# Kernel optimization log

Measured on AMD Instinct MI355X. Metric: run time of the kernel, lower is better.

Reference implementation:

```python
import math
import jax, jax.numpy as jnp
import numpy as np

N, D, K = 8192, 256, 32


def setup_inputs() -> dict:
    key = jax.random.key(0)
    kx, kw, kb = jax.random.split(key, 3)
    x = jax.random.normal(kx, (N, D), dtype=jnp.float32)
    # params per _init_weights: w ~ N(1, 0.01), b ~ N(0, 0.01)
    w = 1.0 + 0.01 * jax.random.normal(kw, (K, D), dtype=jnp.float32)
    b = 0.01 * jax.random.normal(kb, (K, D), dtype=jnp.float32)
    return {"x": x, "w": w, "b": b}


def reference(x, w, b):
    # x: (N, D); w, b: (K, D)
    y1 = w[None, :, :] * (x[:, None, :] + b[None, :, :])        # (N, K, D)
    y2 = y1 * y1                                                 # (N, K, D)
    y4 = -0.5 * jnp.sum(y2, axis=-1)                             # (N, K)
    gamma = jax.nn.softmax(y4, axis=-1)                          # (N, K)
    y6 = (y2 - 1.0) * (1.0 / math.sqrt(2.0))                     # (N, K, D)
    g = gamma[:, :, None]                                        # (N, K, 1)
    n, kk, d = y1.shape
    sigma_part = (g * y6).reshape(n, kk * d)                     # (N, K*D)
    mu_part = (g * y1).reshape(n, kk * d)                        # (N, K*D)
    phi_patches = jnp.concatenate([sigma_part, mu_part], axis=-1)
    return jnp.mean(phi_patches, axis=0)                         # (2*K*D,)
```

## Files before the change

### kernel.cpp

```cpp
#include <hip/hip_runtime.h>
#include <math.h>

#define Nn 8192
#define Dd 256
#define Kk 32

typedef float        f4x __attribute__((ext_vector_type(4)));
typedef unsigned int u2x __attribute__((ext_vector_type(2)));
typedef unsigned int u4x __attribute__((ext_vector_type(4)));

#define P2_OFF  2097152
#define SP_OFF  2228224

__device__ __forceinline__ unsigned bfpack(float a, float b) {
    unsigned ua = __float_as_uint(a); ua += 0x7FFFu + ((ua >> 16) & 1u);
    unsigned ub = __float_as_uint(b); ub += 0x7FFFu + ((ub >> 16) & 1u);
    return (ua >> 16) | (ub & 0xFFFF0000u);
}
__device__ __forceinline__ void nt_store_bf4(unsigned short* p, f4x v) {
    u2x d2; d2.x = bfpack(v.x, v.y); d2.y = bfpack(v.z, v.w);
    __builtin_nontemporal_store(d2, (u2x*)p);
}
__device__ __forceinline__ float bflo(unsigned u) { return __uint_as_float(u << 16); }
__device__ __forceinline__ float bfhi(unsigned u) { return __uint_as_float(u & 0xFFFF0000u); }

__global__ __launch_bounds__(1024) void fused_kernel(const float* __restrict__ x,
                                                     const float* __restrict__ w,
                                                     const float* __restrict__ b,
                                                     float* __restrict__ ws) {
    __shared__ __align__(16) float4 uS4[64 * 33];
    __shared__ __align__(16) float4 vS4[64 * 33];
    __shared__ __align__(16) float4 xS4[32 * 64];
    __shared__ float  gS[1024];

    float* Sp = ws + SP_OFF;
    int tid = threadIdx.x;
    int blk = blockIdx.x;

    {
        const float* xg = x + (size_t)blk * 32 * Dd;
        #pragma unroll
        for (int i = 0; i < 2; ++i) {
            int e4 = tid + i * 1024;
            __builtin_amdgcn_global_load_lds(
                (const __attribute__((address_space(1))) void*)(xg + (size_t)e4 * 4),
                (__attribute__((address_space(3))) void*)(&xS4[e4]),
                16, 0, 0);
        }
    }

    {
        const float4* w4 = (const float4*)w;
        const float4* b4 = (const float4*)b;
        #pragma unroll
        for (int i = 0; i < 2; ++i) {
            int e4 = tid + i * 1024;
            int k  = e4 >> 6;
            int d4 = e4 & 63;
            float4 wv = w4[e4];
            float4 bv = b4[e4];
            float4 vv = {wv.x * bv.x, wv.y * bv.y, wv.z * bv.z, wv.w * bv.w};
            uS4[d4 * 33 + k] = wv;
            vS4[d4 * 33 + k] = vv;
        }
    }
    __syncthreads();

    {
        int lane = tid & 63;
        int wave = tid >> 6;
        int k = lane & 31;
        int h = lane >> 5;
        int r0 = wave * 2;

        const float4* xr0 = &xS4[(r0 + 0) * 64];
        const float4* xr1 = &xS4[(r0 + 1) * 64];

        float4 a0 = {0.f, 0.f, 0.f, 0.f}, a1 = a0;

        #pragma unroll 8
        for (int i = 0; i < 32; ++i) {
            int ii = h * 32 + i;
            float4 u  = uS4[ii * 33 + k];
            float4 v  = vS4[ii * 33 + k];
            float4 x0 = xr0[ii];
            float4 x1 = xr1[ii];
            float y;
            y = fmaf(u.x, x0.x, v.x); a0.x = fmaf(y, y, a0.x);
            y = fmaf(u.y, x0.y, v.y); a0.y = fmaf(y, y, a0.y);
            y = fmaf(u.z, x0.z, v.z); a0.z = fmaf(y, y, a0.z);
            y = fmaf(u.w, x0.w, v.w); a0.w = fmaf(y, y, a0.w);
            y = fmaf(u.x, x1.x, v.x); a1.x = fmaf(y, y, a1.x);
            y = fmaf(u.y, x1.y, v.y); a1.y = fmaf(y, y, a1.y);
            y = fmaf(u.z, x1.z, v.z); a1.z = fmaf(y, y, a1.z);
            y = fmaf(u.w, x1.w, v.w); a1.w = fmaf(y, y, a1.w);
        }

        float s0 = (a0.x + a0.y) + (a0.z + a0.w);
        float s1 = (a1.x + a1.y) + (a1.z + a1.w);
        s0 += __shfl_xor(s0, 32);
        s1 += __shfl_xor(s1, 32);
        float y40 = -0.5f * s0, y41 = -0.5f * s1;

        float m0 = y40, m1 = y41;
        #pragma unroll
        for (int o = 16; o >= 1; o >>= 1) {
            m0 = fmaxf(m0, __shfl_xor(m0, o));
            m1 = fmaxf(m1, __shfl_xor(m1, o));
        }
        float e0 = __expf(y40 - m0), e1 = __expf(y41 - m1);
        float t0 = e0, t1 = e1;
        #pragma unroll
        for (int o = 16; o >= 1; o >>= 1) {
            t0 += __shfl_xor(t0, o);
            t1 += __shfl_xor(t1, o);
        }
        if (h == 0) {
            gS[(r0 + 0) * 32 + k] = e0 / t0;
            gS[(r0 + 1) * 32 + k] = e1 / t1;
        }
    }
    __syncthreads();

    if (tid < 32) {
        float s0 = 0.f, s1 = 0.f, s2 = 0.f, s3 = 0.f;
        #pragma unroll
        for (int r = 0; r < 32; r += 4) {
            s0 += gS[(r + 0) * 32 + tid];
            s1 += gS[(r + 1) * 32 + tid];
            s2 += gS[(r + 2) * 32 + tid];
            s3 += gS[(r + 3) * 32 + tid];
        }
        Sp[tid * 256 + blk] = (s0 + s1) + (s2 + s3);
    }

    {
        int kg = tid >> 6;
        int d4 = tid & 63;
        const f4x* xl4 = (const f4x*)xS4;
        const float2* gS2 = (const float2*)gS;

        f4x aG0 = {0.f, 0.f, 0.f, 0.f}, aH0 = aG0, aG1 = aG0, aH1 = aG0;

        #pragma unroll 4
        for (int r = 0; r < 32; ++r) {
            f4x xv = xl4[r * 64 + d4];
            f4x xx = xv * xv;
            float2 g2 = gS2[r * 16 + kg];
            aG0 += g2.x * xv;  aH0 += g2.x * xx;
            aG1 += g2.y * xv;  aH1 += g2.y * xx;
        }

        unsigned short* Pb = (unsigned short*)ws;
        int k0 = kg * 2, k1 = k0 + 1;
        size_t dd = (size_t)4 * d4;
        nt_store_bf4(Pb + ((size_t)(k0 * 2 + 0) * 256 + blk) * 256 + dd, aG0);
        nt_store_bf4(Pb + ((size_t)(k0 * 2 + 1) * 256 + blk) * 256 + dd, aH0);
        nt_store_bf4(Pb + ((size_t)(k1 * 2 + 0) * 256 + blk) * 256 + dd, aG1);
        nt_store_bf4(Pb + ((size_t)(k1 * 2 + 1) * 256 + blk) * 256 + dd, aH1);
    }
}

__global__ __launch_bounds__(256) void red1_kernel(float* __restrict__ ws) {
    const unsigned short* Pb = (const unsigned short*)ws;
    f4x* P24 = (f4x*)(ws + P2_OFF);
    __shared__ __align__(16) f4x sT[512];
    int tid = threadIdx.x;
    int cb = tid & 31;
    int g  = tid >> 5;

    const u4x* p = (const u4x*)(Pb + ((size_t)blockIdx.x * 32 + g * 4) * 256 + cb * 8);
    f4x a0 = {0.f, 0.f, 0.f, 0.f}, a1 = a0;
    #pragma unroll
    for (int j = 0; j < 4; ++j) {
        u4x v = __builtin_nontemporal_load(&p[(size_t)j * 32]);
        a0.x += bflo(v.x); a0.y += bfhi(v.x); a0.z += bflo(v.y); a0.w += bfhi(v.y);
        a1.x += bflo(v.z); a1.y += bfhi(v.z); a1.z += bflo(v.w); a1.w += bfhi(v.w);
    }
    sT[(g * 32 + cb) * 2 + 0] = a0;
    sT[(g * 32 + cb) * 2 + 1] = a1;
    __syncthreads();

    if (g == 0) {
        f4x s0 = sT[cb * 2], s1 = sT[cb * 2 + 1];
        #pragma unroll
        for (int j = 1; j < 8; ++j) {
            s0 += sT[(j * 32 + cb) * 2 + 0];
            s1 += sT[(j * 32 + cb) * 2 + 1];
        }
        P24[(size_t)blockIdx.x * 64 + cb * 2 + 0] = s0;
        P24[(size_t)blockIdx.x * 64 + cb * 2 + 1] = s1;
    }
}

__global__ __launch_bounds__(256) void red2_kernel(const float* __restrict__ w,
                                                   const float* __restrict__ b,
                                                   const float* __restrict__ ws,
                                                   float* __restrict__ out) {
    const float* P2 = ws + P2_OFF;
    const float* Sp = ws + SP_OFF;
    __shared__ float sred[4];
    int k = blockIdx.x, d = threadIdx.x;

    float sv_part = Sp[k * 256 + d];
    #pragma unroll
    for (int o = 32; o >= 1; o >>= 1) sv_part += __shfl_xor(sv_part, o);
    if ((d & 63) == 0) sred[d >> 6] = sv_part;
    __syncthreads();
    float sv = (sred[0] + sred[1]) + (sred[2] + sred[3]);

    const float* pg = P2 + (size_t)(k * 2 + 0) * 8 * 256 + d;
    const float* ph = P2 + (size_t)(k * 2 + 1) * 8 * 256 + d;
    float Gv = 0.f, Hv = 0.f;
    #pragma unroll
    for (int c = 0; c < 8; ++c) {
        Gv += pg[c * 256];
        Hv += ph[c * 256];
    }

    int idx = k * Dd + d;
    float wv = w[idx], bv = b[idx];
    const float invN = 1.0f / 8192.0f;
    const float c2 = 0.70710678118654752440f * invN;
    float mu = wv * (Gv + bv * sv) * invN;
    float w2 = wv * wv;
    float sg = (w2 * (Hv + 2.0f * bv * Gv + bv * bv * sv) - sv) * c2;
    out[idx] = sg;
    out[Kk * Dd + idx] = mu;
}

extern "C" void kernel_launch(void* const* d_in, const int* in_sizes, int n_in,
                              void* d_out, int out_size, void* d_ws, size_t ws_size,
                              hipStream_t stream) {
    const float* x = (const float*)d_in[0];
    const float* w = (const float*)d_in[1];
    const float* b = (const float*)d_in[2];
    float* out = (float*)d_out;
    float* ws = (float*)d_ws;

    hipLaunchKernelGGL(fused_kernel, dim3(256), dim3(1024), 0, stream, x, w, b, ws);
    hipLaunchKernelGGL(red1_kernel,  dim3(512), dim3(256),  0, stream, ws);
    hipLaunchKernelGGL(red2_kernel,  dim3(32),  dim3(256),  0, stream, w, b, ws, out);
}
```

Before: 78.02 us.

## Merge two reduction kernels into one using atomic accumulation into output

Merges the second-stage reduction and the finalize kernel into a single kernel. Each of the 512 blocks reduces its bf16 partials, applies the per-(k,d) affine epilogue terms, and atomically adds its contribution into the output. The output is zeroed at the start of the fused kernel. This removes one kernel launch and the intermediate P2 round trip. In exchange it adds float atomics with up to 16 contenders per output element, and the summation order becomes nondeterministic.

```diff
diff --git a/kernel.cpp b/kernel.cpp
--- a/kernel.cpp
+++ b/kernel.cpp
@@ -9,7 +9,6 @@
 typedef unsigned int u2x __attribute__((ext_vector_type(2)));
 typedef unsigned int u4x __attribute__((ext_vector_type(4)));
 
-#define P2_OFF  2097152
 #define SP_OFF  2228224
 
 __device__ __forceinline__ unsigned bfpack(float a, float b) {
@@ -27,7 +26,8 @@
 __global__ __launch_bounds__(1024) void fused_kernel(const float* __restrict__ x,
                                                      const float* __restrict__ w,
                                                      const float* __restrict__ b,
-                                                     float* __restrict__ ws) {
+                                                     float* __restrict__ ws,
+                                                     float* __restrict__ out) {
     __shared__ __align__(16) float4 uS4[64 * 33];
     __shared__ __align__(16) float4 vS4[64 * 33];
     __shared__ __align__(16) float4 xS4[32 * 64];
@@ -36,6 +36,8 @@
     float* Sp = ws + SP_OFF;
     int tid = threadIdx.x;
     int blk = blockIdx.x;
+
+    if (tid < 64) out[blk * 64 + tid] = 0.f;
 
     {
         const float* xg = x + (size_t)blk * 32 * Dd;
@@ -161,15 +163,23 @@
     }
 }
 
-__global__ __launch_bounds__(256) void red1_kernel(float* __restrict__ ws) {
+__global__ __launch_bounds__(256) void red_final(const float* __restrict__ w,
+                                                 const float* __restrict__ b,
+                                                 const float* __restrict__ ws,
+                                                 float* __restrict__ out) {
     const unsigned short* Pb = (const unsigned short*)ws;
-    f4x* P24 = (f4x*)(ws + P2_OFF);
+    const float* Sp = ws + SP_OFF;
     __shared__ __align__(16) f4x sT[512];
+    __shared__ float sred[4];
     int tid = threadIdx.x;
     int cb = tid & 31;
     int g  = tid >> 5;
-
-    const u4x* p = (const u4x*)(Pb + ((size_t)blockIdx.x * 32 + g * 4) * 256 + cb * 8);
+    int bid = blockIdx.x;
+    int k  = bid >> 4;
+    int gh = (bid >> 3) & 1;
+    int c  = bid & 7;
+
+    const u4x* p = (const u4x*)(Pb + ((size_t)bid * 32 + g * 4) * 256 + cb * 8);
     f4x a0 = {0.f, 0.f, 0.f, 0.f}, a1 = a0;
     #pragma unroll
     for (int j = 0; j < 4; ++j) {
@@ -181,52 +191,40 @@
     sT[(g * 32 + cb) * 2 + 1] = a1;
     __syncthreads();
 
-    if (g == 0) {
-        f4x s0 = sT[cb * 2], s1 = sT[cb * 2 + 1];
-        #pragma unroll
-        for (int j = 1; j < 8; ++j) {
-            s0 += sT[(j * 32 + cb) * 2 + 0];
-            s1 += sT[(j * 32 + cb) * 2 + 1];
-        }
-        P24[(size_t)blockIdx.x * 64 + cb * 2 + 0] = s0;
-        P24[(size_t)blockIdx.x * 64 + cb * 2 + 1] = s1;
-    }
-}
-
-__global__ __launch_bounds__(256) void red2_kernel(const float* __restrict__ w,
-                                                   const float* __restrict__ b,
-                                                   const float* __restrict__ ws,
-                                                   float* __restrict__ out) {
-    const float* P2 = ws + P2_OFF;
-    const float* Sp = ws + SP_OFF;
-    __shared__ float sred[4];
-    int k = blockIdx.x, d = threadIdx.x;
-
-    float sv_part = Sp[k * 256 + d];
+    int d = tid;
+    const float* sTf = (const float*)sT;
+    float s = 0.f;
     #pragma unroll
-    for (int o = 32; o >= 1; o >>= 1) sv_part += __shfl_xor(sv_part, o);
-    if ((d & 63) == 0) sred[d >> 6] = sv_part;
-    __syncthreads();
-    float sv = (sred[0] + sred[1]) + (sred[2] + sred[3]);
-
-    const float* pg = P2 + (size_t)(k * 2 + 0) * 8 * 256 + d;
-    const float* ph = P2 + (size_t)(k * 2 + 1) * 8 * 256 + d;
-    float Gv = 0.f, Hv = 0.f;
-    #pragma unroll
-    for (int c = 0; c < 8; ++c) {
-        Gv += pg[c * 256];
-        Hv += ph[c * 256];
-    }
+    for (int j = 0; j < 8; ++j) s += sTf[j * 256 + d];
 
     int idx = k * Dd + d;
     float wv = w[idx], bv = b[idx];
     const float invN = 1.0f / 8192.0f;
     const float c2 = 0.70710678118654752440f * invN;
-    float mu = wv * (Gv + bv * sv) * invN;
     float w2 = wv * wv;
-    float sg = (w2 * (Hv + 2.0f * bv * Gv + bv * bv * sv) - sv) * c2;
-    out[idx] = sg;
-    out[Kk * Dd + idx] = mu;
+
+    float sg_c, mu_c;
+    if (gh == 0) {
+        mu_c = wv * s * invN;
+        sg_c = w2 * 2.0f * bv * s * c2;
+    } else {
+        mu_c = 0.f;
+        sg_c = w2 * s * c2;
+    }
+
+    if (gh == 0 && c == 0) {
+        float svp = Sp[k * 256 + tid];
+        #pragma unroll
+        for (int o = 32; o >= 1; o >>= 1) svp += __shfl_xor(svp, o);
+        if ((tid & 63) == 0) sred[tid >> 6] = svp;
+        __syncthreads();
+        float sv = (sred[0] + sred[1]) + (sred[2] + sred[3]);
+        sg_c += (w2 * bv * bv - 1.0f) * sv * c2;
+        mu_c += wv * bv * sv * invN;
+    }
+
+    atomicAdd(&out[idx], sg_c);
+    if (gh == 0) atomicAdd(&out[Kk * Dd + idx], mu_c);
 }
 
 extern "C" void kernel_launch(void* const* d_in, const int* in_sizes, int n_in,
@@ -238,7 +236,6 @@
     float* out = (float*)d_out;
     float* ws = (float*)d_ws;
 
-    hipLaunchKernelGGL(fused_kernel, dim3(256), dim3(1024), 0, stream, x, w, b, ws);
-    hipLaunchKernelGGL(red1_kernel,  dim3(512), dim3(256),  0, stream, ws);
-    hipLaunchKernelGGL(red2_kernel,  dim3(32),  dim3(256),  0, stream, w, b, ws, out);
-}
+    hipLaunchKernelGGL(fused_kernel, dim3(256), dim3(1024), 0, stream, x, w, b, ws, out);
+    hipLaunchKernelGGL(red_final,    dim3(512), dim3(256),  0, stream, w, b, ws, out);
+}
```

After: 76.18 us, median of 2. -2.4%, faster.
